# Kernel optimization log

Measured on AMD Instinct MI355X. Metric: run time of the kernel, lower is better.

The kernel has to match this reference:

```python
import jax, jax.numpy as jnp
import numpy as np

N_NODES = 50000
HEADS = 4
CH = 128
NEG_SLOPE = 0.2


def _gatv2_layer(x, src, dst, Wl, Wr, att, bias):
    # x: [N, Fin]; src/dst: [E'] (self-loops already appended)
    N = x.shape[0]
    xl = (x @ Wl).reshape(N, HEADS, CH)   # source-side transform
    xr = (x @ Wr).reshape(N, HEADS, CH)   # target-side transform
    e = jax.nn.leaky_relu(xl[src] + xr[dst], NEG_SLOPE)   # [E', H, C]
    logits = jnp.einsum('ehc,hc->eh', e, att)             # [E', H]
    # segment softmax over incoming edges of each destination node
    m = jax.ops.segment_max(logits, dst, num_segments=N)
    m = jnp.where(jnp.isfinite(m), m, 0.0)
    p = jnp.exp(logits - m[dst])
    denom = jax.ops.segment_sum(p, dst, num_segments=N)
    alpha = p / denom[dst]                                # [E', H]
    out = jax.ops.segment_sum(alpha[:, :, None] * xl[src], dst, num_segments=N)
    return out.reshape(N, HEADS * CH) + bias


def setup_inputs() -> dict:
    key = jax.random.key(0)
    ks = jax.random.split(key, 12)
    E = 400000
    x = jax.random.normal(ks[0], (N_NODES, 55), dtype=jnp.float32)
    edge_index = jax.random.randint(ks[1], (2, E), 0, N_NODES, dtype=jnp.int64)
    s = 0.1
    d1, d2 = 55, HEADS * CH
    return {
        'x': x,
        'edge_index': edge_index,
        'W1l': jax.random.normal(ks[2], (d1, d2), dtype=jnp.float32) * s,
        'W1r': jax.random.normal(ks[3], (d1, d2), dtype=jnp.float32) * s,
        'att1': jax.random.normal(ks[4], (HEADS, CH), dtype=jnp.float32) * s,
        'b1': jnp.zeros((d2,), dtype=jnp.float32),
        'W2l': jax.random.normal(ks[5], (d2, d2), dtype=jnp.float32) * s,
        'W2r': jax.random.normal(ks[6], (d2, d2), dtype=jnp.float32) * s,
        'att2': jax.random.normal(ks[7], (HEADS, CH), dtype=jnp.float32) * s,
        'b2': jnp.zeros((d2,), dtype=jnp.float32),
        'Wc': jax.random.normal(ks[8], (d2, 49), dtype=jnp.float32) * s,
        'bc': jnp.zeros((49,), dtype=jnp.float32),
    }


def reference(x, edge_index, W1l, W1r, att1, b1, W2l, W2r, att2, b2, Wc, bc):
    # add self loops once (PyG GATv2Conv default add_self_loops=True)
    loops = jnp.arange(N_NODES, dtype=edge_index.dtype)
    src = jnp.concatenate([edge_index[0], loops])
    dst = jnp.concatenate([edge_index[1], loops])
    h = _gatv2_layer(x, src, dst, W1l, W1r, att1, b1)
    h = jax.nn.elu(h)  # dropout is identity in eval mode
    h = _gatv2_layer(h, src, dst, W2l, W2r, att2, b2)
    h = jax.nn.elu(h)
    # forward applies conv2 a second time (conv3 unused in source)
    h = _gatv2_layer(h, src, dst, W2l, W2r, att2, b2)
    h = jax.nn.elu(h)
    return h @ Wc + bc
```

## Files before the change

kernel.cpp:

```cpp
#include <hip/hip_runtime.h>
#include <hip/hip_bf16.h>

constexpr int NN   = 50000;
constexpr int EE   = 400000;
constexpr int EP   = 450000;
constexpr int D    = 512;
constexpr int D2   = 1024;
constexpr int F0   = 55;
constexpr int F0P  = 64;
constexpr int OUTC = 49;

typedef __hip_bfloat16 bf16;

using frag_ab  = __attribute__((ext_vector_type(8))) short;
using frag_cd4 = __attribute__((ext_vector_type(4))) float;
typedef float v2f __attribute__((ext_vector_type(2)));

__device__ inline void stf(float* p, float v) { *p = v; }
__device__ inline void stf(bf16* p, float v)  { *p = __float2bfloat16(v); }

__device__ inline void unpack8v(uint4 u, v2f* f) {
    unsigned w[4] = {u.x, u.y, u.z, u.w};
    #pragma unroll
    for (int j = 0; j < 4; ++j) {
        __hip_bfloat162 h = *(__hip_bfloat162*)&w[j];
        float2 t = __bfloat1622float2(h);
        f[j] = v2f{t.x, t.y};
    }
}

template <typename TC, int NS>
__global__ __launch_bounds__(512, 4) void gemm_dp(
    const bf16* __restrict__ A,
    const bf16* __restrict__ Bt,
    TC* __restrict__ C,
    const float* __restrict__ bias,
    int M, int Ncs)
{
    constexpr int K  = NS * 32;
    constexpr int BM = 256, BN = 128, BK = 32;
    __shared__ __align__(16) bf16 As[3][BM * BK];
    __shared__ __align__(16) bf16 Bs[3][BN * BK];

    int bx = blockIdx.x, by = blockIdx.y;
    if (gridDim.x == 8) {
        int bid = by * 8 + bx;
        bx = (bid >> 3) & 7;
        by = (bid & 7) + ((bid >> 6) << 3);
    }
    if (by * BM >= M) return;

    const int tid = threadIdx.x;
    const int w   = tid >> 6;
    const int l   = tid & 63;
    const int rowBase = by * BM;
    const int colBase = bx * BN;

    const bf16* gA[2];
    #pragma unroll
    for (int j = 0; j < 2; ++j) {
        int f = j * 512 + tid;
        int row = f >> 2, c = (f & 3) ^ ((row >> 1) & 3);
        int ar = rowBase + row; if (ar >= M) ar = M - 1;
        gA[j] = A + (size_t)ar * K + c * 8;
    }
    const bf16* gB;
    {
        int f = tid;
        int row = f >> 2, c = (f & 3) ^ ((row >> 1) & 3);
        gB = Bt + (size_t)(colBase + row) * K + c * 8;
    }

    const int l15 = l & 15, l4 = l >> 4;
    const int wm = (w >> 1) * 64;
    const int wn = (w & 1) * 64;
    int aoff[4], boff[4];
    #pragma unroll
    for (int i = 0; i < 4; ++i) {
        int ra = wm + i * 16 + l15;
        int rb = wn + i * 16 + l15;
        aoff[i] = ra * BK + ((l4 ^ ((ra >> 1) & 3)) * 8);
        boff[i] = rb * BK + ((l4 ^ ((rb >> 1) & 3)) * 8);
    }

    frag_cd4 acc[4][4] = {};

    auto stage = [&](int s) {
        int slot = s % 3;
        __builtin_amdgcn_global_load_lds(
            (const __attribute__((address_space(1))) void*)(gA[0] + s * BK),
            (__attribute__((address_space(3))) void*)(&As[slot][(w * 64) * 8]),
            16, 0, 0);
        __builtin_amdgcn_global_load_lds(
            (const __attribute__((address_space(1))) void*)(gA[1] + s * BK),
            (__attribute__((address_space(3))) void*)(&As[slot][(512 + w * 64) * 8]),
            16, 0, 0);
        __builtin_amdgcn_global_load_lds(
            (const __attribute__((address_space(1))) void*)(gB + s * BK),
            (__attribute__((address_space(3))) void*)(&Bs[slot][(w * 64) * 8]),
            16, 0, 0);
    };

    stage(0);
    if (NS > 1) stage(1);

    #pragma unroll
    for (int s = 0; s < NS; ++s) {
        if (s + 1 < NS) asm volatile("s_waitcnt vmcnt(3)" ::: "memory");
        else            asm volatile("s_waitcnt vmcnt(0)" ::: "memory");
        __builtin_amdgcn_s_barrier();
        asm volatile("" ::: "memory");

        if (s + 2 < NS) stage(s + 2);

        const bf16* Ab = As[s % 3];
        const bf16* Bb = Bs[s % 3];
        frag_ab a[4], b[4];
        #pragma unroll
        for (int i = 0; i < 4; ++i) a[i] = *(const frag_ab*)&Ab[aoff[i]];
        #pragma unroll
        for (int n = 0; n < 4; ++n) b[n] = *(const frag_ab*)&Bb[boff[n]];

        __builtin_amdgcn_s_setprio(1);
        #pragma unroll
        for (int i = 0; i < 4; ++i)
            #pragma unroll
            for (int n = 0; n < 4; ++n)
                acc[i][n] = __builtin_amdgcn_mfma_f32_16x16x32_bf16(
                    a[i], b[n], acc[i][n], 0, 0, 0);
        __builtin_amdgcn_s_setprio(0);
    }

    #pragma unroll
    for (int mi = 0; mi < 4; ++mi) {
        #pragma unroll
        for (int r = 0; r < 4; ++r) {
            int row = rowBase + wm + mi * 16 + l4 * 4 + r;
            if (row >= M) continue;
            #pragma unroll
            for (int ni = 0; ni < 4; ++ni) {
                int col = colBase + wn + ni * 16 + l15;
                if (col >= Ncs) continue;
                float v = acc[mi][ni][r];
                if (bias) v += bias[col];
                stf(&C[(size_t)row * Ncs + col], v);
            }
        }
    }
}

__global__ void convert_transpose2(const float* __restrict__ W0,
                                   const float* __restrict__ W1,
                                   bf16* __restrict__ Wt) {
    __shared__ float tile[32][33];
    const float* W = blockIdx.z ? W1 : W0;
    bf16* dst = Wt + (size_t)blockIdx.z * D * D;
    int bn = blockIdx.x * 32, bk = blockIdx.y * 32;
    int tx = threadIdx.x & 31, ty = threadIdx.x >> 5;
    #pragma unroll
    for (int i = 0; i < 32; i += 8)
        tile[ty + i][tx] = W[(size_t)(bk + ty + i) * D + bn + tx];
    __syncthreads();
    #pragma unroll
    for (int i = 0; i < 32; i += 8)
        dst[(size_t)(bn + ty + i) * D + bk + tx] = __float2bfloat16(tile[tx][ty + i]);
}

__global__ void pad_convert_x(const float* __restrict__ x, bf16* __restrict__ Xp) {
    int idx = blockIdx.x * blockDim.x + threadIdx.x;
    if (idx >= NN * F0P) return;
    int n = idx >> 6, t = idx & 63;
    float v = (t < F0) ? x[n * F0 + t] : 0.f;
    Xp[idx] = __float2bfloat16(v);
}

__global__ void conv_transpose_w1(const float* __restrict__ Wl,
                                  const float* __restrict__ Wr,
                                  bf16* __restrict__ Wt) {
    const float* W = blockIdx.y ? Wr : Wl;
    bf16* dst = Wt + (size_t)blockIdx.y * D * F0P;
    int n = blockIdx.x;
    int k = threadIdx.x;
    float v = (k < F0) ? W[(size_t)k * D + n] : 0.f;
    dst[n * F0P + k] = __float2bfloat16(v);
}

__global__ void conv_transpose_wc(const float* __restrict__ W, bf16* __restrict__ Wt) {
    int n = blockIdx.x;
    for (int k = threadIdx.x; k < D; k += blockDim.x) {
        float v = (n < OUTC) ? W[(size_t)k * OUTC + n] : 0.f;
        Wt[(size_t)n * D + k] = __float2bfloat16(v);
    }
}

__global__ void zero_ints(int* __restrict__ p, int n) {
    int i = blockIdx.x * blockDim.x + threadIdx.x;
    if (i < n) p[i] = 0;
}

__global__ void count_dst(const int* __restrict__ dstIdx, int* __restrict__ cnt) {
    int e = blockIdx.x * blockDim.x + threadIdx.x;
    if (e >= EP) return;
    int dst = (e < EE) ? dstIdx[e] : (e - EE);
    atomicAdd(&cnt[dst], 1);
}

__global__ void scan_blocks(const int* __restrict__ cnt, int* __restrict__ off,
                            int* __restrict__ bsum) {
    __shared__ int sh[1024];
    int i = blockIdx.x * 1024 + threadIdx.x;
    int v = (i < NN) ? cnt[i] : 0;
    sh[threadIdx.x] = v;
    __syncthreads();
    #pragma unroll
    for (int d = 1; d < 1024; d <<= 1) {
        int t = (threadIdx.x >= d) ? sh[threadIdx.x - d] : 0;
        __syncthreads();
        sh[threadIdx.x] += t;
        __syncthreads();
    }
    if (i < NN) off[i] = sh[threadIdx.x] - v;
    if (threadIdx.x == 1023) bsum[blockIdx.x] = sh[1023];
}

__global__ void scan_bsums(int* __restrict__ bsum, int* __restrict__ bbase,
                           int* __restrict__ off, int nb) {
    int lane = threadIdx.x;
    int orig = (lane < nb) ? bsum[lane] : 0;
    int v = orig;
    #pragma unroll
    for (int d = 1; d < 64; d <<= 1) {
        int t = __shfl_up(v, d);
        if (lane >= d) v += t;
    }
    if (lane < nb) bbase[lane] = v - orig;
    if (lane == 63) off[NN] = v;
}

__global__ void add_base(int* __restrict__ off, const int* __restrict__ bbase) {
    int i = blockIdx.x * 1024 + threadIdx.x;
    if (blockIdx.x == 0 || i >= NN) return;
    off[i] += bbase[blockIdx.x];
}

__global__ void fill_srcpos(const int* __restrict__ srcIdx, const int* __restrict__ dstIdx,
                            const int* __restrict__ off, int* __restrict__ cnt,
                            int* __restrict__ srcPos) {
    int e = blockIdx.x * blockDim.x + threadIdx.x;
    if (e >= EP) return;
    int dst = (e < EE) ? dstIdx[e] : (e - EE);
    int src = (e < EE) ? srcIdx[e] : (e - EE);
    int pos = off[dst] + atomicAdd(&cnt[dst], 1);
    srcPos[pos] = src;
}

__global__ __launch_bounds__(256) void gat_edge_fused(
    const bf16* __restrict__ XLR, const float* __restrict__ att,
    const int* __restrict__ off, const int* __restrict__ srcPos,
    const float* __restrict__ bias, bf16* __restrict__ Hout)
{
    int v = blockIdx.x * 4 + (threadIdx.x >> 6);
    if (v >= NN) return;
    int lane = threadIdx.x & 63;

    uint4 ru = *(const uint4*)(XLR + (size_t)v * D2 + D + lane * 8);
    v2f xr[4]; unpack8v(ru, xr);
    const float4* a4 = (const float4*)(att + lane * 8);
    float4 aa = a4[0], ab = a4[1];
    v2f at[4] = {v2f{aa.x, aa.y}, v2f{aa.z, aa.w},
                 v2f{ab.x, ab.y}, v2f{ab.z, ab.w}};
    const v2f k02 = {0.2f, 0.2f};

    int s0 = off[v], s1 = off[v + 1];
    float den = 0.f;
    v2f acc[4] = {v2f{0.f, 0.f}, v2f{0.f, 0.f}, v2f{0.f, 0.f}, v2f{0.f, 0.f}};

    uint4 lb0 = {0, 0, 0, 0}, lb1 = {0, 0, 0, 0};
    if (s0 < s1)     lb0 = *(const uint4*)(XLR + (size_t)srcPos[s0] * D2 + lane * 8);
    if (s0 + 1 < s1) lb1 = *(const uint4*)(XLR + (size_t)srcPos[s0 + 1] * D2 + lane * 8);

    for (int i = s0; i < s1; ++i) {
        uint4 cur = lb0;
        lb0 = lb1;
        if (i + 2 < s1)
            lb1 = *(const uint4*)(XLR + (size_t)srcPos[i + 2] * D2 + lane * 8);

        v2f xl[4]; unpack8v(cur, xl);
        v2f s2 = {0.f, 0.f};
        #pragma unroll
        for (int j = 0; j < 4; ++j) {
            v2f t = xl[j] + xr[j];
            v2f u = t * k02;
            t.x = fmaxf(t.x, u.x);
            t.y = fmaxf(t.y, u.y);
            s2 = t * at[j] + s2;
        }
        float s = s2.x + s2.y;
        s += __shfl_xor(s, 1);
        s += __shfl_xor(s, 2);
        s += __shfl_xor(s, 4);
        s += __shfl_xor(s, 8);
        s = fminf(fmaxf(s, -60.f), 60.f);
        float p = __expf(s);
        den += p;
        v2f pv = {p, p};
        #pragma unroll
        for (int j = 0; j < 4; ++j) acc[j] = xl[j] * pv + acc[j];
    }
    float r = 1.f / den;
    v2f rv = {r, r};

    const float4* b4 = (const float4*)(bias + lane * 8);
    float4 ba = b4[0], bb = b4[1];
    v2f bi[4] = {v2f{ba.x, ba.y}, v2f{ba.z, ba.w},
                 v2f{bb.x, bb.y}, v2f{bb.z, bb.w}};
    uint4 ou;
    unsigned* ow = (unsigned*)&ou;
    #pragma unroll
    for (int j = 0; j < 4; ++j) {
        v2f o = acc[j] * rv + bi[j];
        float o0 = o.x > 0.f ? o.x : (__expf(o.x) - 1.f);
        float o1 = o.y > 0.f ? o.y : (__expf(o.y) - 1.f);
        __hip_bfloat162 h{__float2bfloat16(o0), __float2bfloat16(o1)};
        ow[j] = *(unsigned*)&h;
    }
    *(uint4*)(Hout + (size_t)v * D + lane * 8) = ou;
}

extern "C" void kernel_launch(void* const* d_in, const int* in_sizes, int n_in,
                              void* d_out, int out_size, void* d_ws, size_t ws_size,
                              hipStream_t stream) {
    const float* x    = (const float*)d_in[0];
    const int*   ei   = (const int*)d_in[1];
    const float* W1l  = (const float*)d_in[2];
    const float* W1r  = (const float*)d_in[3];
    const float* att1 = (const float*)d_in[4];
    const float* b1   = (const float*)d_in[5];
    const float* W2l  = (const float*)d_in[6];
    const float* W2r  = (const float*)d_in[7];
    const float* att2 = (const float*)d_in[8];
    const float* b2   = (const float*)d_in[9];
    const float* Wc   = (const float*)d_in[10];
    const float* bc   = (const float*)d_in[11];
    float* out = (float*)d_out;

    const int* srcIdx = ei;
    const int* dstIdx = ei + EE;

    constexpr int NB = (NN + 1023) / 1024;

    bf16* XLR  = (bf16*)d_ws;
    bf16* Hb   = XLR + (size_t)NN * D2;
    bf16* Xpad = Hb + (size_t)NN * D;
    bf16* W2T  = Xpad + (size_t)NN * F0P;
    bf16* W1T  = W2T + (size_t)D2 * D;
    bf16* WcT  = W1T + (size_t)D2 * F0P;
    int* cnt   = (int*)(WcT + (size_t)128 * D);
    int* cnt2  = cnt + NN;
    int* off   = cnt2 + NN;
    int* srcPos= off + (NN + 1);
    int* bsum  = srcPos + EP;
    int* bbase = bsum + NB;

    zero_ints<<<(2 * NN + 255) / 256, 256, 0, stream>>>(cnt, 2 * NN);
    count_dst<<<(EP + 255) / 256, 256, 0, stream>>>(dstIdx, cnt);
    scan_blocks<<<NB, 1024, 0, stream>>>(cnt, off, bsum);
    scan_bsums<<<1, 64, 0, stream>>>(bsum, bbase, off, NB);
    add_base<<<NB, 1024, 0, stream>>>(off, bbase);
    fill_srcpos<<<(EP + 255) / 256, 256, 0, stream>>>(srcIdx, dstIdx, off, cnt2, srcPos);

    dim3 ctGrid(D / 32, D / 32, 2);
    convert_transpose2<<<ctGrid, 256, 0, stream>>>(W2l, W2r, W2T);
    dim3 w1Grid(D, 2);
    conv_transpose_w1<<<w1Grid, F0P, 0, stream>>>(W1l, W1r, W1T);
    conv_transpose_wc<<<128, 256, 0, stream>>>(Wc, WcT);
    pad_convert_x<<<(NN * F0P + 255) / 256, 256, 0, stream>>>(x, Xpad);

    int panels = (NN + 255) / 256;
    int gy = (panels + 7) / 8 * 8;
    dim3 gemmGrid(D2 / 128, gy);
    int nodeBlocks = (NN + 3) / 4;

    gemm_dp<bf16, 2><<<gemmGrid, 512, 0, stream>>>(Xpad, W1T, XLR, nullptr, NN, D2);
    gat_edge_fused<<<nodeBlocks, 256, 0, stream>>>(XLR, att1, off, srcPos, b1, Hb);

    for (int rep = 0; rep < 2; ++rep) {
        gemm_dp<bf16, 16><<<gemmGrid, 512, 0, stream>>>(Hb, W2T, XLR, nullptr, NN, D2);
        gat_edge_fused<<<nodeBlocks, 256, 0, stream>>>(XLR, att2, off, srcPos, b2, Hb);
    }

    dim3 gridc(1, panels);
    gemm_dp<float, 16><<<gridc, 512, 0, stream>>>(Hb, WcT, out, bc, NN, OUTC);
}
```

Baseline: 575.8 us.

## Sort nodes by degree and split edge aggregation per head across quarter-waves

Builds a degree-bucketed permutation of destination nodes (histogram, scan, scatter) so that nodes with similar in-degree share a wavefront, which reduces loop-trip divergence. The edge kernel now assigns one attention head to each 16-lane group, so each wave processes four nodes for a single head, and blocks are interleaved across heads. This adds three small preprocessing kernels and more blocks. Gathers per node become 256-byte head slices, which may lower coalescing efficiency.

```diff
diff --git a/kernel.cpp b/kernel.cpp
--- a/kernel.cpp
+++ b/kernel.cpp
@@ -254,18 +254,52 @@
     srcPos[pos] = src;
 }
 
-__global__ __launch_bounds__(256) void gat_edge_fused(
+__global__ void hist_deg(const int* __restrict__ cnt, int* __restrict__ hist) {
+    int v = blockIdx.x * blockDim.x + threadIdx.x;
+    if (v >= NN) return;
+    atomicAdd(&hist[min(cnt[v], 63)], 1);
+}
+
+__global__ void scan_hist(int* __restrict__ hist) {
+    int lane = threadIdx.x;
+    int orig = hist[lane];
+    int v = orig;
+    #pragma unroll
+    for (int d = 1; d < 64; d <<= 1) {
+        int t = __shfl_up(v, d);
+        if (lane >= d) v += t;
+    }
+    hist[lane] = v - orig;
+}
+
+__global__ void scatter_perm(const int* __restrict__ cnt, int* __restrict__ hist,
+                             int* __restrict__ perm) {
+    int v = blockIdx.x * blockDim.x + threadIdx.x;
+    if (v >= NN) return;
+    int r = atomicAdd(&hist[min(cnt[v], 63)], 1);
+    perm[r] = v;
+}
+
+__global__ __launch_bounds__(256) void gat_edge_head(
     const bf16* __restrict__ XLR, const float* __restrict__ att,
     const int* __restrict__ off, const int* __restrict__ srcPos,
-    const float* __restrict__ bias, bf16* __restrict__ Hout)
+    const int* __restrict__ perm, const float* __restrict__ bias,
+    bf16* __restrict__ Hout)
 {
-    int v = blockIdx.x * 4 + (threadIdx.x >> 6);
-    if (v >= NN) return;
+    int bid = blockIdx.x;
+    int h   = (bid & 7) >> 1;
+    int nb  = ((bid >> 3) << 1) + (bid & 1);
+    if (nb >= NN / 16) return;
     int lane = threadIdx.x & 63;
-
-    uint4 ru = *(const uint4*)(XLR + (size_t)v * D2 + D + lane * 8);
+    int grp  = lane >> 4;
+    int l16  = lane & 15;
+    int rank = nb * 16 + (int)(threadIdx.x >> 6) * 4 + grp;
+    int v = perm[rank];
+    const int hoff = h * 128 + l16 * 8;
+
+    uint4 ru = *(const uint4*)(XLR + (size_t)v * D2 + D + hoff);
     v2f xr[4]; unpack8v(ru, xr);
-    const float4* a4 = (const float4*)(att + lane * 8);
+    const float4* a4 = (const float4*)(att + hoff);
     float4 aa = a4[0], ab = a4[1];
     v2f at[4] = {v2f{aa.x, aa.y}, v2f{aa.z, aa.w},
                  v2f{ab.x, ab.y}, v2f{ab.z, ab.w}};
@@ -276,14 +310,14 @@
     v2f acc[4] = {v2f{0.f, 0.f}, v2f{0.f, 0.f}, v2f{0.f, 0.f}, v2f{0.f, 0.f}};
 
     uint4 lb0 = {0, 0, 0, 0}, lb1 = {0, 0, 0, 0};
-    if (s0 < s1)     lb0 = *(const uint4*)(XLR + (size_t)srcPos[s0] * D2 + lane * 8);
-    if (s0 + 1 < s1) lb1 = *(const uint4*)(XLR + (size_t)srcPos[s0 + 1] * D2 + lane * 8);
+    if (s0 < s1)     lb0 = *(const uint4*)(XLR + (size_t)srcPos[s0] * D2 + hoff);
+    if (s0 + 1 < s1) lb1 = *(const uint4*)(XLR + (size_t)srcPos[s0 + 1] * D2 + hoff);
 
     for (int i = s0; i < s1; ++i) {
         uint4 cur = lb0;
         lb0 = lb1;
         if (i + 2 < s1)
-            lb1 = *(const uint4*)(XLR + (size_t)srcPos[i + 2] * D2 + lane * 8);
+            lb1 = *(const uint4*)(XLR + (size_t)srcPos[i + 2] * D2 + hoff);
 
         v2f xl[4]; unpack8v(cur, xl);
         v2f s2 = {0.f, 0.f};
@@ -310,7 +344,7 @@
     float r = 1.f / den;
     v2f rv = {r, r};
 
-    const float4* b4 = (const float4*)(bias + lane * 8);
+    const float4* b4 = (const float4*)(bias + hoff);
     float4 ba = b4[0], bb = b4[1];
     v2f bi[4] = {v2f{ba.x, ba.y}, v2f{ba.z, ba.w},
                  v2f{bb.x, bb.y}, v2f{bb.z, bb.w}};
@@ -321,10 +355,10 @@
         v2f o = acc[j] * rv + bi[j];
         float o0 = o.x > 0.f ? o.x : (__expf(o.x) - 1.f);
         float o1 = o.y > 0.f ? o.y : (__expf(o.y) - 1.f);
-        __hip_bfloat162 h{__float2bfloat16(o0), __float2bfloat16(o1)};
-        ow[j] = *(unsigned*)&h;
-    }
-    *(uint4*)(Hout + (size_t)v * D + lane * 8) = ou;
+        __hip_bfloat162 hh{__float2bfloat16(o0), __float2bfloat16(o1)};
+        ow[j] = *(unsigned*)&hh;
+    }
+    *(uint4*)(Hout + (size_t)v * D + hoff) = ou;
 }
 
 extern "C" void kernel_launch(void* const* d_in, const int* in_sizes, int n_in,
@@ -357,17 +391,22 @@
     bf16* WcT  = W1T + (size_t)D2 * F0P;
     int* cnt   = (int*)(WcT + (size_t)128 * D);
     int* cnt2  = cnt + NN;
-    int* off   = cnt2 + NN;
+    int* hist  = cnt2 + NN;
+    int* off   = hist + 64;
     int* srcPos= off + (NN + 1);
     int* bsum  = srcPos + EP;
     int* bbase = bsum + NB;
-
-    zero_ints<<<(2 * NN + 255) / 256, 256, 0, stream>>>(cnt, 2 * NN);
+    int* perm  = bbase + NB;
+
+    zero_ints<<<(2 * NN + 64 + 255) / 256, 256, 0, stream>>>(cnt, 2 * NN + 64);
     count_dst<<<(EP + 255) / 256, 256, 0, stream>>>(dstIdx, cnt);
     scan_blocks<<<NB, 1024, 0, stream>>>(cnt, off, bsum);
     scan_bsums<<<1, 64, 0, stream>>>(bsum, bbase, off, NB);
     add_base<<<NB, 1024, 0, stream>>>(off, bbase);
     fill_srcpos<<<(EP + 255) / 256, 256, 0, stream>>>(srcIdx, dstIdx, off, cnt2, srcPos);
+    hist_deg<<<(NN + 255) / 256, 256, 0, stream>>>(cnt, hist);
+    scan_hist<<<1, 64, 0, stream>>>(hist);
+    scatter_perm<<<(NN + 255) / 256, 256, 0, stream>>>(cnt, hist, perm);
 
     dim3 ctGrid(D / 32, D / 32, 2);
     convert_transpose2<<<ctGrid, 256, 0, stream>>>(W2l, W2r, W2T);
@@ -379,14 +418,14 @@
     int panels = (NN + 255) / 256;
     int gy = (panels + 7) / 8 * 8;
     dim3 gemmGrid(D2 / 128, gy);
-    int nodeBlocks = (NN + 3) / 4;
+    int headBlocks = 12504;
 
     gemm_dp<bf16, 2><<<gemmGrid, 512, 0, stream>>>(Xpad, W1T, XLR, nullptr, NN, D2);
-    gat_edge_fused<<<nodeBlocks, 256, 0, stream>>>(XLR, att1, off, srcPos, b1, Hb);
+    gat_edge_head<<<headBlocks, 256, 0, stream>>>(XLR, att1, off, srcPos, perm, b1, Hb);
 
     for (int rep = 0; rep < 2; ++rep) {
         gemm_dp<bf16, 16><<<gemmGrid, 512, 0, stream>>>(Hb, W2T, XLR, nullptr, NN, D2);
-        gat_edge_fused<<<nodeBlocks, 256, 0, stream>>>(XLR, att2, off, srcPos, b2, Hb);
+        gat_edge_head<<<headBlocks, 256, 0, stream>>>(XLR, att2, off, srcPos, perm, b2, Hb);
     }
 
     dim3 gridc(1, panels);
```

Result: slower. 916.7 us (+59.2%).
